# Optimization experiments

Hardware: AMD Instinct MI355X
Metric: run time of the kernel (lower is better)

The kernel has to match this reference:

```python
import jax, jax.numpy as jnp
import numpy as np

BLOCK_SIZE = 1024
QMIN, QMAX = 0, 255          # bit=8, asymmetric
GAMMA, ZETA = -0.1, 1.1      # rectified-sigmoid bounds
K_OUTLIER = 3.0              # outlier threshold in std units


def setup_inputs() -> dict:
    key = jax.random.key(0)
    k1, k2, k3 = jax.random.split(key, 3)
    X = jax.random.normal(k1, (4096, 11008), dtype=jnp.float32) * 0.02
    n_blocks = X.size // BLOCK_SIZE  # 44032
    # positive per-block scales, realistic magnitude for 8-bit weight quant
    scale = jax.random.uniform(k2, (n_blocks, 1), dtype=jnp.float32,
                               minval=0.0005, maxval=0.002)
    alpha = jax.random.normal(k3, (n_blocks, BLOCK_SIZE), dtype=jnp.float32)
    return {"X": X, "scale": scale, "alpha": alpha, "zero_point": 128}


def reference(X, scale, alpha, zero_point):
    zp = jnp.float32(zero_point)
    # flatten_into_blocks: [n_blocks, block_size]
    blocks = X.reshape(-1, BLOCK_SIZE)
    # rectified sigmoid soft rounding offset in [0, 1]
    h = jnp.clip((ZETA - GAMMA) * jax.nn.sigmoid(alpha) + GAMMA, 0.0, 1.0)
    Xq = jnp.floor(blocks / scale) + h + zp
    Xq = jnp.clip(Xq, QMIN, QMAX)
    Xd = (Xq - zp) * scale
    # reconstruct_from_blocks
    x_out = Xd.reshape(X.shape)
    # outlier mask: |X - mean| > k*std; extract/restore == keep original values there
    mu = jnp.mean(X)
    sd = jnp.std(X)
    mask = jnp.abs(X - mu) > K_OUTLIER * sd
    return jnp.where(mask, X, x_out)
```

## Files before the change

### kernel.cpp

```cpp
#include <hip/hip_runtime.h>
#include <math.h>


constexpr int RED_BLOCKS  = 2048;
constexpr int RED_THREADS = 256;

__global__ __launch_bounds__(RED_THREADS)
void stats_partial_kernel(const float4* __restrict__ x4,
                          double2* __restrict__ part, int n4) {
    double s = 0.0, ss = 0.0;
    const int stride = gridDim.x * blockDim.x;
    for (int i = blockIdx.x * blockDim.x + threadIdx.x; i < n4; i += stride) {
        float4 v = x4[i];
        double vx = v.x, vy = v.y, vz = v.z, vw = v.w;
        s  += (vx + vy) + (vz + vw);
        ss += (vx * vx + vy * vy) + (vz * vz + vw * vw);
    }
    for (int off = 32; off > 0; off >>= 1) {
        s  += __shfl_down(s,  off, 64);
        ss += __shfl_down(ss, off, 64);
    }
    __shared__ double sh[8];
    const int wave = threadIdx.x >> 6;
    if ((threadIdx.x & 63) == 0) { sh[wave * 2] = s; sh[wave * 2 + 1] = ss; }
    __syncthreads();
    if (threadIdx.x == 0) {
        double ts = 0.0, tss = 0.0;
        for (int w = 0; w < (RED_THREADS >> 6); ++w) {
            ts += sh[w * 2]; tss += sh[w * 2 + 1];
        }
        part[blockIdx.x] = make_double2(ts, tss);
    }
}

__global__ __launch_bounds__(256)
void stats_final_kernel(const double2* __restrict__ part, int nparts,
                        float2* __restrict__ stats, long long n) {
    double s = 0.0, ss = 0.0;
    for (int i = threadIdx.x; i < nparts; i += blockDim.x) {
        double2 p = part[i];
        s += p.x; ss += p.y;
    }
    for (int off = 32; off > 0; off >>= 1) {
        s  += __shfl_down(s,  off, 64);
        ss += __shfl_down(ss, off, 64);
    }
    __shared__ double sh[8];
    const int wave = threadIdx.x >> 6;
    if ((threadIdx.x & 63) == 0) { sh[wave * 2] = s; sh[wave * 2 + 1] = ss; }
    __syncthreads();
    if (threadIdx.x == 0) {
        double ts = 0.0, tss = 0.0;
        for (int w = 0; w < 4; ++w) { ts += sh[w * 2]; tss += sh[w * 2 + 1]; }
        double mu  = ts / (double)n;
        double var = tss / (double)n - mu * mu;
        float  sdf = (float)sqrt(fmax(var, 0.0));
        stats->x = (float)mu;
        stats->y = 3.0f * sdf;
    }
}

__global__ __launch_bounds__(256)
void quant_kernel(const float4* __restrict__ x4,
                  const float*  __restrict__ scale,
                  const float4* __restrict__ a4,
                  const int*    __restrict__ zp_ptr,
                  const float2* __restrict__ stats,
                  float4* __restrict__ out4) {
    const int i  = blockIdx.x * 256 + threadIdx.x;
    const float s   = scale[blockIdx.x];
    const float inv_s = 1.0f / s;
    (void)inv_s;
    const float zp  = (float)(*zp_ptr);
    const float2 st = *stats;
    const float mu  = st.x;
    const float thr = st.y;

    float4 x = x4[i];
    float4 a = a4[i];
    float4 o;

    #pragma unroll
    for (int c = 0; c < 4; ++c) {
        float xc = (&x.x)[c];
        float ac = (&a.x)[c];
        float sig = 1.0f / (1.0f + __expf(-ac));
        float h   = fminf(fmaxf(1.2f * sig - 0.1f, 0.0f), 1.0f);
        float xq  = floorf(xc / s) + h + zp;
        xq        = fminf(fmaxf(xq, 0.0f), 255.0f);
        float xd  = (xq - zp) * s;
        (&o.x)[c] = (fabsf(xc - mu) > thr) ? xc : xd;
    }
    out4[i] = o;
}

extern "C" void kernel_launch(void* const* d_in, const int* in_sizes, int n_in,
                              void* d_out, int out_size, void* d_ws, size_t ws_size,
                              hipStream_t stream) {
    const float* X     = (const float*)d_in[0];
    const float* scale = (const float*)d_in[1];
    const float* alpha = (const float*)d_in[2];
    const int*   zp    = (const int*)d_in[3];
    float* out         = (float*)d_out;

    const int n  = in_sizes[0];
    const int n4 = n / 4;
    const int qblocks = n / 1024;

    double2* part  = (double2*)d_ws;
    float2*  stats = (float2*)(part + RED_BLOCKS);

    stats_partial_kernel<<<RED_BLOCKS, RED_THREADS, 0, stream>>>(
        (const float4*)X, part, n4);
    stats_final_kernel<<<1, 256, 0, stream>>>(part, RED_BLOCKS, stats, (long long)n);
    quant_kernel<<<qblocks, 256, 0, stream>>>(
        (const float4*)X, scale, (const float4*)alpha, zp, stats,
        (float4*)out);
}
```

Before: 425.6 us.

## Process two quant blocks per thread, use nontemporal loads/stores and reciprocal scale

The quant kernel now handles two 1024-element blocks per workgroup, so each thread issues two independent vector loads, which increases memory-level parallelism. Alpha loads and output stores use nontemporal builtins to avoid polluting the cache with streaming data. Division by scale is replaced by multiplication with a precomputed reciprocal. The reciprocal can change floor results by one ulp near integer boundaries, and halving the grid size may reduce occupancy.

```diff
diff --git a/kernel.cpp b/kernel.cpp
--- a/kernel.cpp
+++ b/kernel.cpp
@@ -1,17 +1,19 @@
 #include <hip/hip_runtime.h>
 #include <math.h>
 
+
+typedef float f32x4 __attribute__((ext_vector_type(4)));
 
 constexpr int RED_BLOCKS  = 2048;
 constexpr int RED_THREADS = 256;
 
 __global__ __launch_bounds__(RED_THREADS)
-void stats_partial_kernel(const float4* __restrict__ x4,
+void stats_partial_kernel(const f32x4* __restrict__ x4,
                           double2* __restrict__ part, int n4) {
     double s = 0.0, ss = 0.0;
     const int stride = gridDim.x * blockDim.x;
     for (int i = blockIdx.x * blockDim.x + threadIdx.x; i < n4; i += stride) {
-        float4 v = x4[i];
+        f32x4 v = x4[i];
         double vx = v.x, vy = v.y, vz = v.z, vw = v.w;
         s  += (vx + vy) + (vz + vw);
         ss += (vx * vx + vy * vy) + (vz * vz + vw * vw);
@@ -55,43 +57,60 @@
         double mu  = ts / (double)n;
         double var = tss / (double)n - mu * mu;
         float  sdf = (float)sqrt(fmax(var, 0.0));
-        stats->x = (float)mu;
-        stats->y = 3.0f * sdf;
+        float2 st;
+        st.x = (float)mu;
+        st.y = 3.0f * sdf;
+        *stats = st;
     }
 }
 
 __global__ __launch_bounds__(256)
-void quant_kernel(const float4* __restrict__ x4,
-                  const float*  __restrict__ scale,
-                  const float4* __restrict__ a4,
-                  const int*    __restrict__ zp_ptr,
+void quant_kernel(const f32x4* __restrict__ x4,
+                  const float* __restrict__ scale,
+                  const f32x4* __restrict__ a4,
+                  const int*   __restrict__ zp_ptr,
                   const float2* __restrict__ stats,
-                  float4* __restrict__ out4) {
-    const int i  = blockIdx.x * 256 + threadIdx.x;
-    const float s   = scale[blockIdx.x];
-    const float inv_s = 1.0f / s;
-    (void)inv_s;
-    const float zp  = (float)(*zp_ptr);
+                  f32x4* __restrict__ out4) {
+    const int t = threadIdx.x;
+    const long long base = (long long)blockIdx.x * 512;
+    const float s0 = scale[blockIdx.x * 2];
+    const float s1 = scale[blockIdx.x * 2 + 1];
+    const float r0 = 1.0f / s0;
+    const float r1 = 1.0f / s1;
+    const float zp = (float)(*zp_ptr);
     const float2 st = *stats;
     const float mu  = st.x;
     const float thr = st.y;
 
-    float4 x = x4[i];
-    float4 a = a4[i];
-    float4 o;
+    f32x4 x0 = x4[base + t];
+    f32x4 x1 = x4[base + 256 + t];
+    f32x4 a0 = __builtin_nontemporal_load(&a4[base + t]);
+    f32x4 a1 = __builtin_nontemporal_load(&a4[base + 256 + t]);
 
+    f32x4 o0, o1;
     #pragma unroll
     for (int c = 0; c < 4; ++c) {
-        float xc = (&x.x)[c];
-        float ac = (&a.x)[c];
-        float sig = 1.0f / (1.0f + __expf(-ac));
-        float h   = fminf(fmaxf(1.2f * sig - 0.1f, 0.0f), 1.0f);
-        float xq  = floorf(xc / s) + h + zp;
-        xq        = fminf(fmaxf(xq, 0.0f), 255.0f);
-        float xd  = (xq - zp) * s;
-        (&o.x)[c] = (fabsf(xc - mu) > thr) ? xc : xd;
+        {
+            float xc = x0[c], ac = a0[c];
+            float sig = 1.0f / (1.0f + __expf(-ac));
+            float h   = fminf(fmaxf(1.2f * sig - 0.1f, 0.0f), 1.0f);
+            float xq  = floorf(xc * r0) + h + zp;
+            xq        = fminf(fmaxf(xq, 0.0f), 255.0f);
+            float xd  = (xq - zp) * s0;
+            o0[c] = (fabsf(xc - mu) > thr) ? xc : xd;
+        }
+        {
+            float xc = x1[c], ac = a1[c];
+            float sig = 1.0f / (1.0f + __expf(-ac));
+            float h   = fminf(fmaxf(1.2f * sig - 0.1f, 0.0f), 1.0f);
+            float xq  = floorf(xc * r1) + h + zp;
+            xq        = fminf(fmaxf(xq, 0.0f), 255.0f);
+            float xd  = (xq - zp) * s1;
+            o1[c] = (fabsf(xc - mu) > thr) ? xc : xd;
+        }
     }
-    out4[i] = o;
+    __builtin_nontemporal_store(o0, &out4[base + t]);
+    __builtin_nontemporal_store(o1, &out4[base + 256 + t]);
 }
 
 extern "C" void kernel_launch(void* const* d_in, const int* in_sizes, int n_in,
@@ -105,15 +124,15 @@
 
     const int n  = in_sizes[0];
     const int n4 = n / 4;
-    const int qblocks = n / 1024;
+    const int qpairs = n / 2048;
 
     double2* part  = (double2*)d_ws;
     float2*  stats = (float2*)(part + RED_BLOCKS);
 
     stats_partial_kernel<<<RED_BLOCKS, RED_THREADS, 0, stream>>>(
-        (const float4*)X, part, n4);
+        (const f32x4*)X, part, n4);
     stats_final_kernel<<<1, 256, 0, stream>>>(part, RED_BLOCKS, stats, (long long)n);
-    quant_kernel<<<qblocks, 256, 0, stream>>>(
-        (const float4*)X, scale, (const float4*)alpha, zp, stats,
-        (float4*)out);
+    quant_kernel<<<qpairs, 256, 0, stream>>>(
+        (const f32x4*)X, scale, (const f32x4*)alpha, zp, stats,
+        (f32x4*)out);
 }
```

Measured after the change: 417.4 us. No clear change (-1.9%).
